# Kernel tuning notes

Measured on AMD Instinct MI355X. Metric: run time of the kernel, lower is better.

The kernel has to match this reference:

```python
import jax, jax.numpy as jnp
import numpy as np

B, S, D, E = 16, 2048, 1024, 524288

def setup_inputs() -> dict:
    key = jax.random.key(0)
    k0, k1, k2, k3 = jax.random.split(key, 4)
    x = jax.random.normal(k0, (B, S, D), dtype=jnp.float32)
    mask = jnp.ones((B, S), dtype=bool)
    edges = jax.random.randint(k1, (2, E), 0, B * S, dtype=jnp.int32)
    scale = 1.0 / np.sqrt(D).astype(np.float32)
    W1 = jax.random.normal(k2, (D, D), dtype=jnp.float32) * scale  # GCNConv lin weight
    b1 = jnp.zeros((D,), dtype=jnp.float32)                        # GCNConv bias
    W2 = jax.random.normal(k3, (D, D), dtype=jnp.float32) * scale  # output Linear
    b2 = jnp.zeros((D,), dtype=jnp.float32)
    return {"x": x, "mask": mask, "edges": edges, "W1": W1, "b1": b1, "W2": W2, "b2": b2}

def reference(x, mask, edges, W1, b1, W2, b2):
    # x: [B,S,D]; mask all-True -> gather == reshape to [N,D]
    N = B * S
    nodes = x.reshape(N, D)
    src, dst = edges[0], edges[1]
    # GCN normalization (gcn_norm, add_self_loops=False): deg over dst, norm = d^-1/2[src]*d^-1/2[dst]
    deg = jax.ops.segment_sum(jnp.ones((E,), dtype=nodes.dtype), dst, num_segments=N)
    dinv = jnp.where(deg > 0, jax.lax.rsqrt(jnp.maximum(deg, 1e-12)), 0.0)
    norm = dinv[src] * dinv[dst]  # [E]
    h = nodes @ W1.T                                   # [N,D] transform
    msg = h[src] * norm[:, None]                       # [E,D] gather + scale
    agg = jax.ops.segment_sum(msg, dst, num_segments=N) + b1  # scatter-aggregate + bias
    g = jax.nn.gelu(agg, approximate=False)            # nn.GELU (exact erf)
    out = g @ W2.T + b2                                # Linear(graph_hid_dim -> input_dim)
    # residual scatter-add back into x (mask all True)
    return x + (out.reshape(B, S, D) * mask[:, :, None].astype(x.dtype))
```

## Files before the change

### kernel.cpp

```cpp
#include <hip/hip_runtime.h>
#include <hip/hip_fp8.h>
#include <stdint.h>

typedef unsigned short u16;
typedef __attribute__((ext_vector_type(8))) short s16x8;
typedef __attribute__((ext_vector_type(4))) float f32x4;
typedef __attribute__((ext_vector_type(2))) float f32x2;

#define D_DIM 1024
#define GK 1024
#define NT 16

__device__ __forceinline__ u16 f2bf(float f) {
  union { float f; uint32_t u; } v; v.f = f;
  uint32_t u = v.u;
  return (u16)((u + 0x7FFFu + ((u >> 16) & 1u)) >> 16);
}
__device__ __forceinline__ float bf2f(u16 b) {
  union { uint32_t u; float f; } v; v.u = ((uint32_t)b) << 16;
  return v.f;
}

__device__ __forceinline__ uint8_t f2fp8(float f) {
#if __has_builtin(__builtin_amdgcn_cvt_pk_fp8_f32)
  int p = __builtin_amdgcn_cvt_pk_fp8_f32(f, f, 0, false);
  return (uint8_t)(p & 0xff);
#else
  return __hip_fp8_e4m3(f).__x;
#endif
}


__device__ __forceinline__ int lds_half_off(int arr, int buf, int half) {
  return ((((arr << 1) | buf) << 1) | half) << 14;
}

__device__ __forceinline__ void stage_half(const u16* __restrict__ g, int rowBase, int kt,
                                           u16* lds, int arr, int buf, int half, int t) {
  const int hoff = lds_half_off(arr, buf, half);
#pragma unroll
  for (int j = 0; j < 2; ++j) {
    const int c = j * 512 + t;
    const int row = c >> 3;
    const int cb = (((c & 7) ^ (row & 7)) << 4);
    const u16* src = g + (size_t)(rowBase + half * 128 + row) * GK + kt * 64 + (cb >> 1);
    __builtin_amdgcn_global_load_lds((const __attribute__((address_space(1))) void*)src,
        (__attribute__((address_space(3))) void*)((char*)lds + hoff + c * 16), 16, 0, 0);
  }
}

template<int QM>
__device__ __forceinline__ void read_sub_a(const u16* lds, int buf, int half, int lane, s16x8* a) {
  const int base = lds_half_off(0, buf, half);
  const int rsel = lane & 15, cb0 = (lane >> 4) << 4;
#pragma unroll
  for (int im = 0; im < 4; ++im) {
    const int row = QM * 64 + im * 16 + rsel;
    const int swz = (row & 7) << 4;
#pragma unroll
    for (int ks = 0; ks < 2; ++ks)
      a[im * 2 + ks] = *(const s16x8*)((const char*)lds + base + row * 128 + ((ks * 64 + cb0) ^ swz));
  }
}

template<int QN>
__device__ __forceinline__ void read_sub_b(const u16* lds, int buf, int half, int rowBase, int lane, s16x8* b) {
  const int base = lds_half_off(1, buf, half);
  const int rsel = lane & 15, cb0 = (lane >> 4) << 4;
#pragma unroll
  for (int in_ = 0; in_ < 2; ++in_) {
    const int row = rowBase + (QN * 2 + in_) * 16 + rsel;
    const int swz = (row & 7) << 4;
#pragma unroll
    for (int ks = 0; ks < 2; ++ks)
      b[in_ * 2 + ks] = *(const s16x8*)((const char*)lds + base + row * 128 + ((ks * 64 + cb0) ^ swz));
  }
}

template<int QM, int QN>
__device__ __forceinline__ void do_quad(f32x4 acc[8][4], const s16x8* aS, const s16x8* bS) {
  __builtin_amdgcn_s_setprio(1);
#pragma unroll
  for (int im = 0; im < 4; ++im)
#pragma unroll
    for (int in_ = 0; in_ < 2; ++in_)
#pragma unroll
      for (int ks = 0; ks < 2; ++ks)
        acc[QM * 4 + im][QN * 2 + in_] = __builtin_amdgcn_mfma_f32_16x16x32_bf16(
            aS[im * 2 + ks], bS[in_ * 2 + ks], acc[QM * 4 + im][QN * 2 + in_], 0, 0, 0);
  __builtin_amdgcn_s_setprio(0);
}

#define BARRIER __builtin_amdgcn_s_barrier()
#define WAIT_LGKM asm volatile("s_waitcnt lgkmcnt(0)" ::: "memory")
#define WAIT_VM(n) asm volatile("s_waitcnt vmcnt(" #n ")" ::: "memory")

template<int EPI>
__global__ __launch_bounds__(512, 2) void gemm256(
    const u16* __restrict__ A, const u16* __restrict__ B, uint8_t* __restrict__ C8,
    const float* __restrict__ bias, const u16* __restrict__ xres, float* __restrict__ Cf)
{
  __shared__ u16 lds[65536];
  const int t = threadIdx.x;
  const int lane = t & 63;
  const int w = t >> 6;
  const int wave_m = w >> 2;
  const int wave_n = w & 3;
  const int halfB = wave_n >> 1;
  const int rowBaseB = (wave_n & 1) * 64;

  const int lb = blockIdx.x;
  const int wid = ((lb & 7) << 6) | (lb >> 3);
  const int bm = wid >> 2;
  const int bn = wid & 3;
  const int rowA = bm * 256;
  const int rowB = bn * 256;

  f32x4 acc[8][4] = {};
  s16x8 aS[8], b0S[4], b1S[4];

  stage_half(A, rowA, 0, lds, 0, 0, 0, t);
  stage_half(A, rowA, 0, lds, 0, 0, 1, t);
  stage_half(B, rowB, 0, lds, 1, 0, 0, t);
  stage_half(B, rowB, 0, lds, 1, 0, 1, t);
  stage_half(B, rowB, 1, lds, 1, 1, 0, t);
  stage_half(B, rowB, 1, lds, 1, 1, 1, t);
  WAIT_VM(4);
  BARRIER;

  for (int i = 0; i < NT / 2 - 1; ++i) {
    const int t1 = 2 * i + 1;
    read_sub_a<0>(lds, 0, wave_m, lane, aS);
    read_sub_b<0>(lds, 0, halfB, rowBaseB, lane, b0S);
    stage_half(A, rowA, t1, lds, 0, 1, 0, t);
    BARRIER; WAIT_LGKM;
    do_quad<0, 0>(acc, aS, b0S);
    BARRIER;
    read_sub_b<1>(lds, 0, halfB, rowBaseB, lane, b1S);
    stage_half(A, rowA, t1, lds, 0, 1, 1, t);
    BARRIER; WAIT_LGKM;
    do_quad<0, 1>(acc, aS, b1S);
    BARRIER;
    read_sub_a<1>(lds, 0, wave_m, lane, aS);
    stage_half(B, rowB, 2 * i + 2, lds, 1, 0, 0, t);
    BARRIER; WAIT_LGKM;
    do_quad<1, 1>(acc, aS, b1S);
    BARRIER;
    stage_half(B, rowB, 2 * i + 2, lds, 1, 0, 1, t);
    WAIT_VM(4);
    BARRIER;
    do_quad<1, 0>(acc, aS, b0S);
    BARRIER;
    read_sub_a<0>(lds, 1, wave_m, lane, aS);
    read_sub_b<0>(lds, 1, halfB, rowBaseB, lane, b0S);
    stage_half(A, rowA, 2 * i + 2, lds, 0, 0, 0, t);
    BARRIER; WAIT_LGKM;
    do_quad<0, 0>(acc, aS, b0S);
    BARRIER;
    read_sub_b<1>(lds, 1, halfB, rowBaseB, lane, b1S);
    stage_half(A, rowA, 2 * i + 2, lds, 0, 0, 1, t);
    BARRIER; WAIT_LGKM;
    do_quad<0, 1>(acc, aS, b1S);
    BARRIER;
    read_sub_a<1>(lds, 1, wave_m, lane, aS);
    stage_half(B, rowB, 2 * i + 3, lds, 1, 1, 0, t);
    BARRIER; WAIT_LGKM;
    do_quad<1, 1>(acc, aS, b1S);
    BARRIER;
    stage_half(B, rowB, 2 * i + 3, lds, 1, 1, 1, t);
    WAIT_VM(4);
    BARRIER;
    do_quad<1, 0>(acc, aS, b0S);
    BARRIER;
  }

  {
    read_sub_a<0>(lds, 0, wave_m, lane, aS);
    read_sub_b<0>(lds, 0, halfB, rowBaseB, lane, b0S);
    stage_half(A, rowA, NT - 1, lds, 0, 1, 0, t);
    BARRIER; WAIT_LGKM;
    do_quad<0, 0>(acc, aS, b0S);
    BARRIER;
    read_sub_b<1>(lds, 0, halfB, rowBaseB, lane, b1S);
    stage_half(A, rowA, NT - 1, lds, 0, 1, 1, t);
    BARRIER; WAIT_LGKM;
    do_quad<0, 1>(acc, aS, b1S);
    BARRIER;
    read_sub_a<1>(lds, 0, wave_m, lane, aS);
    BARRIER; WAIT_LGKM;
    do_quad<1, 1>(acc, aS, b1S);
    BARRIER;
    WAIT_VM(0);
    BARRIER;
    do_quad<1, 0>(acc, aS, b0S);
    read_sub_a<0>(lds, 1, wave_m, lane, aS);
    read_sub_b<0>(lds, 1, halfB, rowBaseB, lane, b0S);
    WAIT_LGKM;
    do_quad<0, 0>(acc, aS, b0S);
    read_sub_b<1>(lds, 1, halfB, rowBaseB, lane, b1S);
    WAIT_LGKM;
    do_quad<0, 1>(acc, aS, b1S);
    read_sub_a<1>(lds, 1, wave_m, lane, aS);
    WAIT_LGKM;
    do_quad<1, 1>(acc, aS, b1S);
    do_quad<1, 0>(acc, aS, b0S);
  }

  const int row0 = rowA + wave_m * 128 + ((lane >> 4) << 2);
  const int col0 = rowB + wave_n * 64 + (lane & 15);
  if (EPI == 0) {
#pragma unroll
    for (int mf = 0; mf < 8; ++mf)
#pragma unroll
      for (int nf = 0; nf < 4; ++nf) {
        const int c = col0 + nf * 16;
#pragma unroll
        for (int r = 0; r < 4; ++r)
          C8[(size_t)(row0 + mf * 16 + r) * D_DIM + c] = f2fp8(acc[mf][nf][r]);
      }
  } else {
#pragma unroll
    for (int mf = 0; mf < 8; ++mf)
#pragma unroll
      for (int nf = 0; nf < 4; ++nf) {
        const int c = col0 + nf * 16;
        const float bv = bias[c];
#pragma unroll
        for (int r = 0; r < 4; ++r) {
          const size_t idx = (size_t)(row0 + mf * 16 + r) * D_DIM + c;
          Cf[idx] = acc[mf][nf][r] + bv + bf2f(xres[idx]);
        }
      }
  }
}

__global__ void cast_f32_bf16(const float* __restrict__ in, u16* __restrict__ out, long n) {
  long i = ((long)blockIdx.x * blockDim.x + threadIdx.x) * 4;
  if (i >= n) return;
  const float4 v = *(const float4*)(in + i);
  ushort4 o;
  o.x = f2bf(v.x); o.y = f2bf(v.y); o.z = f2bf(v.z); o.w = f2bf(v.w);
  *(ushort4*)(out + i) = o;
}

__global__ void deg_count_int(const int* __restrict__ dst, int* __restrict__ cnt, int E) {
  int i = blockIdx.x * blockDim.x + threadIdx.x;
  if (i < E) atomicAdd(&cnt[dst[i]], 1);
}

__global__ __launch_bounds__(1024) void scan_offsets(const int* __restrict__ cnt,
                                                     int* __restrict__ off,
                                                     int* __restrict__ cursor,
                                                     float* __restrict__ dinv, int N) {
  __shared__ int part[1024];
  const int t = threadIdx.x;
  const int nper = (N + 1023) / 1024;
  const int base = t * nper;
  int s = 0;
  for (int i = 0; i < nper; ++i) {
    int idx = base + i;
    if (idx < N) s += cnt[idx];
  }
  part[t] = s;
  __syncthreads();
  for (int d = 1; d < 1024; d <<= 1) {
    int v = (t >= d) ? part[t - d] : 0;
    __syncthreads();
    part[t] += v;
    __syncthreads();
  }
  int run = (t > 0) ? part[t - 1] : 0;
  for (int i = 0; i < nper; ++i) {
    int idx = base + i;
    if (idx < N) {
      const int c = cnt[idx];
      off[idx] = run;
      cursor[idx] = run;
      dinv[idx] = c > 0 ? rsqrtf((float)c) : 0.f;
      run += c;
    }
  }
  if (t == 1023) off[N] = run;
}

__global__ void fill_csr(const int* __restrict__ src, const int* __restrict__ dst,
                         const float* __restrict__ dinv, int* __restrict__ cursor,
                         uint2* __restrict__ ebuf, int E) {
  int e = blockIdx.x * blockDim.x + threadIdx.x;
  if (e >= E) return;
  const int d = dst[e], s = src[e];
  const int pos = atomicAdd(&cursor[d], 1);
  const float nrm = dinv[s] * dinv[d];
  uint2 en; en.x = (unsigned)s; en.y = __float_as_uint(nrm);
  ebuf[pos] = en;
}

__device__ __forceinline__ void acc8_fp8(float* a, uint2 hv, float nrm) {
#if __has_builtin(__builtin_amdgcn_cvt_pk_f32_fp8)
  const f32x2 p0 = __builtin_amdgcn_cvt_pk_f32_fp8(hv.x, false);
  const f32x2 p1 = __builtin_amdgcn_cvt_pk_f32_fp8(hv.x, true);
  const f32x2 p2 = __builtin_amdgcn_cvt_pk_f32_fp8(hv.y, false);
  const f32x2 p3 = __builtin_amdgcn_cvt_pk_f32_fp8(hv.y, true);
  a[0] += p0.x * nrm; a[1] += p0.y * nrm;
  a[2] += p1.x * nrm; a[3] += p1.y * nrm;
  a[4] += p2.x * nrm; a[5] += p2.y * nrm;
  a[6] += p3.x * nrm; a[7] += p3.y * nrm;
#else
  const float s = nrm * 0x1p+120f;
#pragma unroll
  for (int k = 0; k < 8; ++k) {
    const uint32_t word = (k < 4) ? hv.x : hv.y;
    const uint32_t b = (word >> ((k & 3) * 8)) & 0xffu;
    a[k] += __uint_as_float(((b & 0x80u) << 24) | ((b & 0x7fu) << 20)) * s;
  }
#endif
}

__device__ __forceinline__ float gelu_exact(float t) {
  return 0.5f * t * (1.0f + erff(t * 0.70710678118f));
}

__global__ __launch_bounds__(256) void aggregate_gelu_fp8(
    const uint8_t* __restrict__ h8, const uint2* __restrict__ ebuf,
    const int* __restrict__ off, const float* __restrict__ b1,
    u16* __restrict__ g)
{
  const int node = __builtin_amdgcn_readfirstlane(blockIdx.x * 2 + (threadIdx.x >> 7));
  const int lt = threadIdx.x & 127;
  const int fb = lt * 8;
  const int beg = off[node], end = off[node + 1];
  float a[8] = {0.f, 0.f, 0.f, 0.f, 0.f, 0.f, 0.f, 0.f};

  int i = beg;
  for (; i + 2 <= end; i += 2) {
    const uint2 ea = ebuf[i];
    const uint2 eb = ebuf[i + 1];
    const uint2 ha = *(const uint2*)(h8 + (size_t)ea.x * D_DIM + fb);
    const uint2 hb = *(const uint2*)(h8 + (size_t)eb.x * D_DIM + fb);
    acc8_fp8(a, ha, __uint_as_float(ea.y));
    acc8_fp8(a, hb, __uint_as_float(eb.y));
  }
  if (i < end) {
    const uint2 ea = ebuf[i];
    const uint2 ha = *(const uint2*)(h8 + (size_t)ea.x * D_DIM + fb);
    acc8_fp8(a, ha, __uint_as_float(ea.y));
  }

  const float4 bA = *(const float4*)(b1 + fb);
  const float4 bB = *(const float4*)(b1 + fb + 4);
  const float v0 = gelu_exact(a[0] + bA.x), v1 = gelu_exact(a[1] + bA.y);
  const float v2 = gelu_exact(a[2] + bA.z), v3 = gelu_exact(a[3] + bA.w);
  const float v4 = gelu_exact(a[4] + bB.x), v5 = gelu_exact(a[5] + bB.y);
  const float v6 = gelu_exact(a[6] + bB.z), v7 = gelu_exact(a[7] + bB.w);
  uint4 o;
  o.x = (uint32_t)f2bf(v0) | ((uint32_t)f2bf(v1) << 16);
  o.y = (uint32_t)f2bf(v2) | ((uint32_t)f2bf(v3) << 16);
  o.z = (uint32_t)f2bf(v4) | ((uint32_t)f2bf(v5) << 16);
  o.w = (uint32_t)f2bf(v6) | ((uint32_t)f2bf(v7) << 16);
  *(uint4*)(g + (size_t)node * D_DIM + fb) = o;
}

extern "C" void kernel_launch(void* const* d_in, const int* in_sizes, int n_in,
                              void* d_out, int out_size, void* d_ws, size_t ws_size,
                              hipStream_t stream) {
  const float* x  = (const float*)d_in[0];
  const int* edges = (const int*)d_in[2];
  const float* W1 = (const float*)d_in[3];
  const float* b1 = (const float*)d_in[4];
  const float* W2 = (const float*)d_in[5];
  const float* b2 = (const float*)d_in[6];
  float* out = (float*)d_out;

  const int D = D_DIM;
  const long ND = (long)in_sizes[0];
  const int N = (int)(ND / D);
  const int E = in_sizes[2] / 2;
  const int* src = edges;
  const int* dst = edges + E;

  u16* xbf    = (u16*)d_ws;
  u16* gbf    = xbf + ND;
  uint8_t* h8 = (uint8_t*)(gbf + ND);
  u16* w1b    = (u16*)(h8 + ND);
  u16* w2b    = w1b + (size_t)D * D;
  int* cnt    = (int*)(w2b + (size_t)D * D);
  int* off    = cnt + N;
  int* cursor = off + N + 1;
  float* dnv  = (float*)(cursor + N);
  uint2* ebuf = (uint2*)(dnv + N + 1);

  hipMemsetAsync(cnt, 0, (size_t)N * sizeof(int), stream);

  cast_f32_bf16<<<(int)(ND / 4 / 256), 256, 0, stream>>>(x, xbf, ND);
  cast_f32_bf16<<<(int)((long)D * D / 4 / 256), 256, 0, stream>>>(W1, w1b, (long)D * D);
  cast_f32_bf16<<<(int)((long)D * D / 4 / 256), 256, 0, stream>>>(W2, w2b, (long)D * D);

  deg_count_int<<<(E + 255) / 256, 256, 0, stream>>>(dst, cnt, E);
  scan_offsets<<<1, 1024, 0, stream>>>(cnt, off, cursor, dnv, N);
  fill_csr<<<(E + 255) / 256, 256, 0, stream>>>(src, dst, dnv, cursor, ebuf, E);

  gemm256<0><<<(N / 256) * (D / 256), 512, 0, stream>>>(xbf, w1b, h8, nullptr, nullptr, nullptr);

  aggregate_gelu_fp8<<<N / 2, 256, 0, stream>>>(h8, ebuf, off, b1, gbf);

  gemm256<1><<<(N / 256) * (D / 256), 512, 0, stream>>>(gbf, w2b, nullptr, b2, xbf, out);
}
```

Before: 437.5 us.

## Make GEMMs persistent over two tiles per block and merge cast kernels

The two GEMM kernels now launch 256 blocks, and each block computes two 256x256 output tiles one after the other instead of one tile per block. This removes the second wave of blocks on a GPU with 256 CUs, at the cost of serialising two tiles within each block with a barrier between them. The three fp32-to-bf16 cast launches are also merged into one grid-stride kernel to save launch overhead. Neither change overlaps the epilogue of the first tile with the loads for the second.

```diff
diff --git a/kernel.cpp b/kernel.cpp
--- a/kernel.cpp
+++ b/kernel.cpp
@@ -94,6 +94,131 @@
 #define BARRIER __builtin_amdgcn_s_barrier()
 #define WAIT_LGKM asm volatile("s_waitcnt lgkmcnt(0)" ::: "memory")
 #define WAIT_VM(n) asm volatile("s_waitcnt vmcnt(" #n ")" ::: "memory")
+
+template<int EPI>
+__device__ __forceinline__ void gemm_tile_pass(
+    const u16* __restrict__ A, const u16* __restrict__ B, uint8_t* __restrict__ C8,
+    const float* __restrict__ bias, const u16* __restrict__ xres, float* __restrict__ Cf,
+    u16* lds, int rowA, int rowB, int t, int lane, int wave_m, int wave_n,
+    int halfB, int rowBaseB)
+{
+  f32x4 acc[8][4] = {};
+  s16x8 aS[8], b0S[4], b1S[4];
+
+  stage_half(A, rowA, 0, lds, 0, 0, 0, t);
+  stage_half(A, rowA, 0, lds, 0, 0, 1, t);
+  stage_half(B, rowB, 0, lds, 1, 0, 0, t);
+  stage_half(B, rowB, 0, lds, 1, 0, 1, t);
+  stage_half(B, rowB, 1, lds, 1, 1, 0, t);
+  stage_half(B, rowB, 1, lds, 1, 1, 1, t);
+  WAIT_VM(4);
+  BARRIER;
+
+  for (int i = 0; i < NT / 2 - 1; ++i) {
+    const int t1 = 2 * i + 1;
+    read_sub_a<0>(lds, 0, wave_m, lane, aS);
+    read_sub_b<0>(lds, 0, halfB, rowBaseB, lane, b0S);
+    stage_half(A, rowA, t1, lds, 0, 1, 0, t);
+    BARRIER; WAIT_LGKM;
+    do_quad<0, 0>(acc, aS, b0S);
+    BARRIER;
+    read_sub_b<1>(lds, 0, halfB, rowBaseB, lane, b1S);
+    stage_half(A, rowA, t1, lds, 0, 1, 1, t);
+    BARRIER; WAIT_LGKM;
+    do_quad<0, 1>(acc, aS, b1S);
+    BARRIER;
+    read_sub_a<1>(lds, 0, wave_m, lane, aS);
+    stage_half(B, rowB, 2 * i + 2, lds, 1, 0, 0, t);
+    BARRIER; WAIT_LGKM;
+    do_quad<1, 1>(acc, aS, b1S);
+    BARRIER;
+    stage_half(B, rowB, 2 * i + 2, lds, 1, 0, 1, t);
+    WAIT_VM(4);
+    BARRIER;
+    do_quad<1, 0>(acc, aS, b0S);
+    BARRIER;
+    read_sub_a<0>(lds, 1, wave_m, lane, aS);
+    read_sub_b<0>(lds, 1, halfB, rowBaseB, lane, b0S);
+    stage_half(A, rowA, 2 * i + 2, lds, 0, 0, 0, t);
+    BARRIER; WAIT_LGKM;
+    do_quad<0, 0>(acc, aS, b0S);
+    BARRIER;
+    read_sub_b<1>(lds, 1, halfB, rowBaseB, lane, b1S);
+    stage_half(A, rowA, 2 * i + 2, lds, 0, 0, 1, t);
+    BARRIER; WAIT_LGKM;
+    do_quad<0, 1>(acc, aS, b1S);
+    BARRIER;
+    read_sub_a<1>(lds, 1, wave_m, lane, aS);
+    stage_half(B, rowB, 2 * i + 3, lds, 1, 1, 0, t);
+    BARRIER; WAIT_LGKM;
+    do_quad<1, 1>(acc, aS, b1S);
+    BARRIER;
+    stage_half(B, rowB, 2 * i + 3, lds, 1, 1, 1, t);
+    WAIT_VM(4);
+    BARRIER;
+    do_quad<1, 0>(acc, aS, b0S);
+    BARRIER;
+  }
+
+  {
+    read_sub_a<0>(lds, 0, wave_m, lane, aS);
+    read_sub_b<0>(lds, 0, halfB, rowBaseB, lane, b0S);
+    stage_half(A, rowA, NT - 1, lds, 0, 1, 0, t);
+    BARRIER; WAIT_LGKM;
+    do_quad<0, 0>(acc, aS, b0S);
+    BARRIER;
+    read_sub_b<1>(lds, 0, halfB, rowBaseB, lane, b1S);
+    stage_half(A, rowA, NT - 1, lds, 0, 1, 1, t);
+    BARRIER; WAIT_LGKM;
+    do_quad<0, 1>(acc, aS, b1S);
+    BARRIER;
+    read_sub_a<1>(lds, 0, wave_m, lane, aS);
+    BARRIER; WAIT_LGKM;
+    do_quad<1, 1>(acc, aS, b1S);
+    BARRIER;
+    WAIT_VM(0);
+    BARRIER;
+    do_quad<1, 0>(acc, aS, b0S);
+    read_sub_a<0>(lds, 1, wave_m, lane, aS);
+    read_sub_b<0>(lds, 1, halfB, rowBaseB, lane, b0S);
+    WAIT_LGKM;
+    do_quad<0, 0>(acc, aS, b0S);
+    read_sub_b<1>(lds, 1, halfB, rowBaseB, lane, b1S);
+    WAIT_LGKM;
+    do_quad<0, 1>(acc, aS, b1S);
+    read_sub_a<1>(lds, 1, wave_m, lane, aS);
+    WAIT_LGKM;
+    do_quad<1, 1>(acc, aS, b1S);
+    do_quad<1, 0>(acc, aS, b0S);
+  }
+
+  const int row0 = rowA + wave_m * 128 + ((lane >> 4) << 2);
+  const int col0 = rowB + wave_n * 64 + (lane & 15);
+  if (EPI == 0) {
+#pragma unroll
+    for (int mf = 0; mf < 8; ++mf)
+#pragma unroll
+      for (int nf = 0; nf < 4; ++nf) {
+        const int c = col0 + nf * 16;
+#pragma unroll
+        for (int r = 0; r < 4; ++r)
+          C8[(size_t)(row0 + mf * 16 + r) * D_DIM + c] = f2fp8(acc[mf][nf][r]);
+      }
+  } else {
+#pragma unroll
+    for (int mf = 0; mf < 8; ++mf)
+#pragma unroll
+      for (int nf = 0; nf < 4; ++nf) {
+        const int c = col0 + nf * 16;
+        const float bv = bias[c];
+#pragma unroll
+        for (int r = 0; r < 4; ++r) {
+          const size_t idx = (size_t)(row0 + mf * 16 + r) * D_DIM + c;
+          Cf[idx] = acc[mf][nf][r] + bv + bf2f(xres[idx]);
+        }
+      }
+  }
+}
 
 template<int EPI>
 __global__ __launch_bounds__(512, 2) void gemm256(
@@ -108,139 +233,34 @@
   const int wave_n = w & 3;
   const int halfB = wave_n >> 1;
   const int rowBaseB = (wave_n & 1) * 64;
-
   const int lb = blockIdx.x;
-  const int wid = ((lb & 7) << 6) | (lb >> 3);
-  const int bm = wid >> 2;
-  const int bn = wid & 3;
-  const int rowA = bm * 256;
-  const int rowB = bn * 256;
-
-  f32x4 acc[8][4] = {};
-  s16x8 aS[8], b0S[4], b1S[4];
-
-  stage_half(A, rowA, 0, lds, 0, 0, 0, t);
-  stage_half(A, rowA, 0, lds, 0, 0, 1, t);
-  stage_half(B, rowB, 0, lds, 1, 0, 0, t);
-  stage_half(B, rowB, 0, lds, 1, 0, 1, t);
-  stage_half(B, rowB, 1, lds, 1, 1, 0, t);
-  stage_half(B, rowB, 1, lds, 1, 1, 1, t);
-  WAIT_VM(4);
-  BARRIER;
-
-  for (int i = 0; i < NT / 2 - 1; ++i) {
-    const int t1 = 2 * i + 1;
-    read_sub_a<0>(lds, 0, wave_m, lane, aS);
-    read_sub_b<0>(lds, 0, halfB, rowBaseB, lane, b0S);
-    stage_half(A, rowA, t1, lds, 0, 1, 0, t);
-    BARRIER; WAIT_LGKM;
-    do_quad<0, 0>(acc, aS, b0S);
-    BARRIER;
-    read_sub_b<1>(lds, 0, halfB, rowBaseB, lane, b1S);
-    stage_half(A, rowA, t1, lds, 0, 1, 1, t);
-    BARRIER; WAIT_LGKM;
-    do_quad<0, 1>(acc, aS, b1S);
-    BARRIER;
-    read_sub_a<1>(lds, 0, wave_m, lane, aS);
-    stage_half(B, rowB, 2 * i + 2, lds, 1, 0, 0, t);
-    BARRIER; WAIT_LGKM;
-    do_quad<1, 1>(acc, aS, b1S);
-    BARRIER;
-    stage_half(B, rowB, 2 * i + 2, lds, 1, 0, 1, t);
-    WAIT_VM(4);
-    BARRIER;
-    do_quad<1, 0>(acc, aS, b0S);
-    BARRIER;
-    read_sub_a<0>(lds, 1, wave_m, lane, aS);
-    read_sub_b<0>(lds, 1, halfB, rowBaseB, lane, b0S);
-    stage_half(A, rowA, 2 * i + 2, lds, 0, 0, 0, t);
-    BARRIER; WAIT_LGKM;
-    do_quad<0, 0>(acc, aS, b0S);
-    BARRIER;
-    read_sub_b<1>(lds, 1, halfB, rowBaseB, lane, b1S);
-    stage_half(A, rowA, 2 * i + 2, lds, 0, 0, 1, t);
-    BARRIER; WAIT_LGKM;
-    do_quad<0, 1>(acc, aS, b1S);
-    BARRIER;
-    read_sub_a<1>(lds, 1, wave_m, lane, aS);
-    stage_half(B, rowB, 2 * i + 3, lds, 1, 1, 0, t);
-    BARRIER; WAIT_LGKM;
-    do_quad<1, 1>(acc, aS, b1S);
-    BARRIER;
-    stage_half(B, rowB, 2 * i + 3, lds, 1, 1, 1, t);
-    WAIT_VM(4);
-    BARRIER;
-    do_quad<1, 0>(acc, aS, b0S);
-    BARRIER;
-  }
-
-  {
-    read_sub_a<0>(lds, 0, wave_m, lane, aS);
-    read_sub_b<0>(lds, 0, halfB, rowBaseB, lane, b0S);
-    stage_half(A, rowA, NT - 1, lds, 0, 1, 0, t);
-    BARRIER; WAIT_LGKM;
-    do_quad<0, 0>(acc, aS, b0S);
-    BARRIER;
-    read_sub_b<1>(lds, 0, halfB, rowBaseB, lane, b1S);
-    stage_half(A, rowA, NT - 1, lds, 0, 1, 1, t);
-    BARRIER; WAIT_LGKM;
-    do_quad<0, 1>(acc, aS, b1S);
-    BARRIER;
-    read_sub_a<1>(lds, 0, wave_m, lane, aS);
-    BARRIER; WAIT_LGKM;
-    do_quad<1, 1>(acc, aS, b1S);
-    BARRIER;
-    WAIT_VM(0);
-    BARRIER;
-    do_quad<1, 0>(acc, aS, b0S);
-    read_sub_a<0>(lds, 1, wave_m, lane, aS);
-    read_sub_b<0>(lds, 1, halfB, rowBaseB, lane, b0S);
-    WAIT_LGKM;
-    do_quad<0, 0>(acc, aS, b0S);
-    read_sub_b<1>(lds, 1, halfB, rowBaseB, lane, b1S);
-    WAIT_LGKM;
-    do_quad<0, 1>(acc, aS, b1S);
-    read_sub_a<1>(lds, 1, wave_m, lane, aS);
-    WAIT_LGKM;
-    do_quad<1, 1>(acc, aS, b1S);
-    do_quad<1, 0>(acc, aS, b0S);
-  }
-
-  const int row0 = rowA + wave_m * 128 + ((lane >> 4) << 2);
-  const int col0 = rowB + wave_n * 64 + (lane & 15);
-  if (EPI == 0) {
-#pragma unroll
-    for (int mf = 0; mf < 8; ++mf)
-#pragma unroll
-      for (int nf = 0; nf < 4; ++nf) {
-        const int c = col0 + nf * 16;
-#pragma unroll
-        for (int r = 0; r < 4; ++r)
-          C8[(size_t)(row0 + mf * 16 + r) * D_DIM + c] = f2fp8(acc[mf][nf][r]);
-      }
-  } else {
-#pragma unroll
-    for (int mf = 0; mf < 8; ++mf)
-#pragma unroll
-      for (int nf = 0; nf < 4; ++nf) {
-        const int c = col0 + nf * 16;
-        const float bv = bias[c];
-#pragma unroll
-        for (int r = 0; r < 4; ++r) {
-          const size_t idx = (size_t)(row0 + mf * 16 + r) * D_DIM + c;
-          Cf[idx] = acc[mf][nf][r] + bv + bf2f(xres[idx]);
-        }
-      }
-  }
-}
-
-__global__ void cast_f32_bf16(const float* __restrict__ in, u16* __restrict__ out, long n) {
-  long i = ((long)blockIdx.x * blockDim.x + threadIdx.x) * 4;
-  if (i >= n) return;
-  const float4 v = *(const float4*)(in + i);
-  ushort4 o;
-  o.x = f2bf(v.x); o.y = f2bf(v.y); o.z = f2bf(v.z); o.w = f2bf(v.w);
-  *(ushort4*)(out + i) = o;
+
+#pragma unroll
+  for (int p = 0; p < 2; ++p) {
+    const int wid = ((lb & 7) << 6) | ((lb >> 3) + p * 32);
+    const int rowA = (wid >> 2) * 256;
+    const int rowB = (wid & 3) * 256;
+    if (p) BARRIER;
+    gemm_tile_pass<EPI>(A, B, C8, bias, xres, Cf, lds, rowA, rowB,
+                        t, lane, wave_m, wave_n, halfB, rowBaseB);
+  }
+}
+
+__global__ void cast_all_bf16(const float* __restrict__ x, u16* __restrict__ xb, long nx4,
+                              const float* __restrict__ w1, u16* __restrict__ w1b,
+                              const float* __restrict__ w2, u16* __restrict__ w2b, long nw4) {
+  const long total = nx4 + 2 * nw4;
+  for (long i = (long)blockIdx.x * blockDim.x + threadIdx.x; i < total;
+       i += (long)gridDim.x * blockDim.x) {
+    const float* in; u16* out; long j;
+    if (i < nx4) { in = x; out = xb; j = i; }
+    else if (i < nx4 + nw4) { in = w1; out = w1b; j = i - nx4; }
+    else { in = w2; out = w2b; j = i - nx4 - nw4; }
+    const float4 v = *(const float4*)(in + j * 4);
+    ushort4 o;
+    o.x = f2bf(v.x); o.y = f2bf(v.y); o.z = f2bf(v.z); o.w = f2bf(v.w);
+    *(ushort4*)(out + j * 4) = o;
+  }
 }
 
 __global__ void deg_count_int(const int* __restrict__ dst, int* __restrict__ cnt, int E) {
@@ -391,17 +411,15 @@
 
   hipMemsetAsync(cnt, 0, (size_t)N * sizeof(int), stream);
 
-  cast_f32_bf16<<<(int)(ND / 4 / 256), 256, 0, stream>>>(x, xbf, ND);
-  cast_f32_bf16<<<(int)((long)D * D / 4 / 256), 256, 0, stream>>>(W1, w1b, (long)D * D);
-  cast_f32_bf16<<<(int)((long)D * D / 4 / 256), 256, 0, stream>>>(W2, w2b, (long)D * D);
+  cast_all_bf16<<<2048, 256, 0, stream>>>(x, xbf, ND / 4, W1, w1b, W2, w2b, (long)D * D / 4);
 
   deg_count_int<<<(E + 255) / 256, 256, 0, stream>>>(dst, cnt, E);
   scan_offsets<<<1, 1024, 0, stream>>>(cnt, off, cursor, dnv, N);
   fill_csr<<<(E + 255) / 256, 256, 0, stream>>>(src, dst, dnv, cursor, ebuf, E);
 
-  gemm256<0><<<(N / 256) * (D / 256), 512, 0, stream>>>(xbf, w1b, h8, nullptr, nullptr, nullptr);
+  gemm256<0><<<256, 512, 0, stream>>>(xbf, w1b, h8, nullptr, nullptr, nullptr);
 
   aggregate_gelu_fp8<<<N / 2, 256, 0, stream>>>(h8, ebuf, off, b1, gbf);
 
-  gemm256<1><<<(N / 256) * (D / 256), 512, 0, stream>>>(gbf, w2b, nullptr, b2, xbf, out);
-}
+  gemm256<1><<<256, 512, 0, stream>>>(gbf, w2b, nullptr, b2, xbf, out);
+}
```

Result: slower. 455.9 us (+4.2%).
